# Kernel optimization log

Measured on AMD Instinct MI355X. Metric: run time of the kernel, lower is better.

## Reference

```python
import jax, jax.numpy as jnp
import numpy as np

N_GENE, N_CT, N_REF, N_SAMPLE = 50000, 64, 16, 1024

def setup_inputs() -> dict:
    key = jax.random.key(0)
    k1, k2, k3, k4, k5, k6 = jax.random.split(key, 6)
    x = jax.random.normal(k1, (N_GENE * N_CT * N_REF,), dtype=jnp.float32)
    idx = jax.random.randint(k2, (N_CT, N_GENE), 0, N_CT * N_GENE)
    # RefCombLayer weight: uniform around 1/n_ref
    num = 1.0 / N_REF
    w_ref = jax.random.uniform(k3, (N_REF * N_CT,), minval=num - num / 5, maxval=num + num / 5, dtype=jnp.float32)
    # CelltypeScaleLayer weight: normal(1.0, 0.1)
    w_ct = 1.0 + 0.1 * jax.random.normal(k4, (N_CT,), dtype=jnp.float32)
    # StretchLayer weight: normal(1.0, 0.1)
    w_stretch = 1.0 + 0.1 * jax.random.normal(k5, (N_GENE,), dtype=jnp.float32)
    # conv1 kernel: (n_sample, 1, n_kernel), normal(1/n_ct, 0.25/n_ct)
    conv_w = (1.0 / N_CT) + (0.25 / N_CT) * jax.random.normal(k6, (N_SAMPLE, 1, N_CT), dtype=jnp.float32)
    return {"x": x, "idx": idx, "w_ref": w_ref, "w_ct": w_ct,
            "w_stretch": w_stretch, "conv_w": conv_w,
            "N_batch": 1, "N_feature": N_GENE * N_CT}


def reference(x, idx, w_ref, w_ct, w_stretch, conv_w, N_batch, N_feature):
    # RefCombLayer: elementwise mul by per-gene-tiled ref weights
    y = x * jnp.tile(w_ref, N_GENE)                       # [n_gene*n_ct*n_ref]
    # SliceSumLayer: sum over n_ref slices
    y0 = y.reshape(N_CT * N_GENE, N_REF).sum(axis=1)      # [n_ct*n_gene]
    # CelltypeScaleLayer: gather per cell type, scale, flatten transposed
    z = y0[idx] * w_ct[:, None]                           # [n_ct, n_gene]
    y1 = z.T.reshape(-1)                                  # [n_gene*n_ct], gene-major
    # StretchLayer: per-gene weight repeated n_ct times
    y2 = y1 * jnp.repeat(w_stretch, N_CT)                 # [n_gene*n_ct]
    # Conv1d(1, n_sample, kernel=n_ct, stride=n_ct) == per-gene dot with kernel
    yk = y2.reshape(N_GENE, N_CT)                         # [n_gene, n_ct]
    out = jnp.einsum('gk,sk->sg', yk, conv_w[:, 0, :])    # [n_sample, n_gene]
    return (out, y0, y1, y2)
```

## Files before the change

kernel.cpp:

```cpp
#include <hip/hip_runtime.h>

#define NG 50000
#define NCT 64
#define NREF 16
#define NS 1024
#define N0 (NCT * NG)

#define OFF_Y0 ((size_t)NS * NG)
#define OFF_Y1 (OFF_Y0 + N0)
#define OFF_Y2 (OFF_Y1 + N0)

typedef __attribute__((ext_vector_type(8))) short bf16x8;
typedef __attribute__((ext_vector_type(4))) float f32x4;
typedef __attribute__((ext_vector_type(4))) unsigned short u16x4;

__device__ __forceinline__ unsigned short f2bf(float f) {
    union { float f; unsigned u; } v; v.f = f;
    unsigned r = v.u + 0x7fff + ((v.u >> 16) & 1);
    return (unsigned short)(r >> 16);
}
__device__ __forceinline__ float bf2f(unsigned short b) {
    union { float f; unsigned u; } v; v.u = ((unsigned)b) << 16;
    return v.f;
}

__global__ __launch_bounds__(256) void k_y0(const float* __restrict__ x,
                                            const float* __restrict__ w_ref,
                                            float* __restrict__ y0) {
    __shared__ f32x4 wl[256];
    const int tid = threadIdx.x;
    wl[tid] = reinterpret_cast<const f32x4*>(w_ref)[tid];
    __syncthreads();
    const int row = tid & 63;
    const f32x4 w0 = wl[row * 4 + 0];
    const f32x4 w1 = wl[row * 4 + 1];
    const f32x4 w2 = wl[row * 4 + 2];
    const f32x4 w3 = wl[row * 4 + 3];
    const f32x4* x4 = reinterpret_cast<const f32x4*>(x);
    const size_t stride = (size_t)gridDim.x * 256;
    for (size_t j = (size_t)blockIdx.x * 256 + tid; j < (size_t)N0; j += stride) {
        const f32x4* xp = x4 + j * 4;
        f32x4 a = __builtin_nontemporal_load(xp + 0);
        f32x4 b = __builtin_nontemporal_load(xp + 1);
        f32x4 c = __builtin_nontemporal_load(xp + 2);
        f32x4 d = __builtin_nontemporal_load(xp + 3);
        float s = a.x * w0.x + a.y * w0.y + a.z * w0.z + a.w * w0.w
                + b.x * w1.x + b.y * w1.y + b.z * w1.z + b.w * w1.w
                + c.x * w2.x + c.y * w2.y + c.z * w2.z + c.w * w2.w
                + d.x * w3.x + d.y * w3.y + d.z * w3.z + d.w * w3.w;
        y0[j] = s;
    }
}

__global__ __launch_bounds__(256) void k_cw(const float* __restrict__ cw,
                                            unsigned short* __restrict__ cwhi,
                                            unsigned short* __restrict__ cwlo) {
    int i = (blockIdx.x * 256 + threadIdx.x) * 4;
    f32x4 v = *reinterpret_cast<const f32x4*>(cw + i);
    u16x4 h, l;
#pragma unroll
    for (int e = 0; e < 4; ++e) {
        unsigned short hh = f2bf(v[e]);
        h[e] = hh;
        l[e] = f2bf(v[e] - bf2f(hh));
    }
    *reinterpret_cast<u16x4*>(cwhi + i) = h;
    *reinterpret_cast<u16x4*>(cwlo + i) = l;
}

#define STILE 128
template<bool PRECONV>
__global__ __launch_bounds__(256) void k_fused(const float* __restrict__ y0,
                                               const int* __restrict__ idx,
                                               const float* __restrict__ w_ct,
                                               const float* __restrict__ w_stretch,
                                               const float* __restrict__ cw,
                                               const unsigned short* __restrict__ cwhi,
                                               const unsigned short* __restrict__ cwlo,
                                               float* __restrict__ y1,
                                               float* __restrict__ y2,
                                               float* __restrict__ out) {
    __shared__ float T[64 * 65];
    __shared__ unsigned short Yhi[64 * 72];
    __shared__ unsigned short Ylo[64 * 72];

    const int tid = threadIdx.x;
    const int g0 = blockIdx.x * 64;

    int ids[16];
#pragma unroll
    for (int k = 0; k < 16; ++k) {
        int lin = k * 256 + tid;
        int c = lin >> 6, gl = lin & 63;
        int gc = min(g0 + gl, NG - 1);
        ids[k] = idx[c * NG + gc];
    }
    float vals[16];
#pragma unroll
    for (int k = 0; k < 16; ++k) vals[k] = y0[ids[k]];
#pragma unroll
    for (int k = 0; k < 16; ++k) {
        int lin = k * 256 + tid;
        int c = lin >> 6, gl = lin & 63;
        T[c * 65 + gl] = vals[k];
    }
    __syncthreads();

#pragma unroll
    for (int k = 0; k < 16; ++k) {
        int lin = k * 256 + tid;
        int gl = lin >> 6, c = lin & 63;
        int g = g0 + gl;
        float t = T[c * 65 + gl];
        float v1 = t * w_ct[c];
        float v2 = v1 * w_stretch[min(g, NG - 1)];
        int base = gl * 72 + c;
        unsigned short h = f2bf(v2);
        Yhi[base] = h;
        Ylo[base] = f2bf(v2 - bf2f(h));
        if (g < NG) {
            size_t o = (size_t)g * 64 + c;
            __builtin_nontemporal_store(v1, y1 + o);
            __builtin_nontemporal_store(v2, y2 + o);
        }
    }
    __syncthreads();

    const int lane = tid & 63;
    const int wid  = tid >> 6;
    const int l15  = lane & 15;
    const int l4   = lane >> 4;
    const int nb   = wid * 32;

    bf16x8 Ah[4][2], Al[4][2];
#pragma unroll
    for (int m = 0; m < 4; ++m) {
        int grow = m * 16 + l15;
#pragma unroll
        for (int ks = 0; ks < 2; ++ks) {
            int koff = ks * 32 + l4 * 8;
            Ah[m][ks] = *reinterpret_cast<const bf16x8*>(&Yhi[grow * 72 + koff]);
            Al[m][ks] = *reinterpret_cast<const bf16x8*>(&Ylo[grow * 72 + koff]);
        }
    }

    for (int s0 = 0; s0 < NS; s0 += STILE) {
        f32x4 acc[4][2];
#pragma unroll
        for (int m = 0; m < 4; ++m)
#pragma unroll
            for (int n = 0; n < 2; ++n) acc[m][n] = (f32x4){0.f, 0.f, 0.f, 0.f};

#pragma unroll
        for (int n = 0; n < 2; ++n) {
            const size_t srow = (size_t)(s0 + nb + n * 16 + l15) * 64;
            bf16x8 Bh[2], Bl[2];
#pragma unroll
            for (int ks = 0; ks < 2; ++ks) {
                int koff = ks * 32 + l4 * 8;
                if (PRECONV) {
                    Bh[ks] = *reinterpret_cast<const bf16x8*>(cwhi + srow + koff);
                    Bl[ks] = *reinterpret_cast<const bf16x8*>(cwlo + srow + koff);
                } else {
                    f32x4 va = *reinterpret_cast<const f32x4*>(cw + srow + koff);
                    f32x4 vb = *reinterpret_cast<const f32x4*>(cw + srow + koff + 4);
#pragma unroll
                    for (int e = 0; e < 4; ++e) {
                        unsigned short h = f2bf(va[e]);
                        Bh[ks][e] = (short)h;
                        Bl[ks][e] = (short)f2bf(va[e] - bf2f(h));
                        h = f2bf(vb[e]);
                        Bh[ks][e + 4] = (short)h;
                        Bl[ks][e + 4] = (short)f2bf(vb[e] - bf2f(h));
                    }
                }
            }
#pragma unroll
            for (int m = 0; m < 4; ++m)
#pragma unroll
                for (int ks = 0; ks < 2; ++ks) {
                    acc[m][n] = __builtin_amdgcn_mfma_f32_16x16x32_bf16(Ah[m][ks], Bh[ks], acc[m][n], 0, 0, 0);
                    acc[m][n] = __builtin_amdgcn_mfma_f32_16x16x32_bf16(Ah[m][ks], Bl[ks], acc[m][n], 0, 0, 0);
                    acc[m][n] = __builtin_amdgcn_mfma_f32_16x16x32_bf16(Al[m][ks], Bh[ks], acc[m][n], 0, 0, 0);
                }
        }

#pragma unroll
        for (int m = 0; m < 4; ++m) {
            int g4 = g0 + m * 16 + l4 * 4;
            if (g4 < NG) {
#pragma unroll
                for (int n = 0; n < 2; ++n) {
                    int s = s0 + nb + n * 16 + l15;
                    __builtin_nontemporal_store(acc[m][n], reinterpret_cast<f32x4*>(out + (size_t)s * NG + g4));
                }
            }
        }
    }
}

extern "C" void kernel_launch(void* const* d_in, const int* in_sizes, int n_in,
                              void* d_out, int out_size, void* d_ws, size_t ws_size,
                              hipStream_t stream) {
    const float* x         = (const float*)d_in[0];
    const int*   idx       = (const int*)d_in[1];
    const float* w_ref     = (const float*)d_in[2];
    const float* w_ct      = (const float*)d_in[3];
    const float* w_stretch = (const float*)d_in[4];
    const float* conv_w    = (const float*)d_in[5];

    float* out = (float*)d_out;
    float* y0  = out + OFF_Y0;
    float* y1  = out + OFF_Y1;
    float* y2  = out + OFF_Y2;

    k_y0<<<2048, 256, 0, stream>>>(x, w_ref, y0);

    const bool preconv = (ws_size >= (size_t)NS * NCT * 2 * sizeof(unsigned short));
    unsigned short* cwhi = (unsigned short*)d_ws;
    unsigned short* cwlo = cwhi + NS * NCT;
    if (preconv) {
        k_cw<<<NS * NCT / 1024, 256, 0, stream>>>(conv_w, cwhi, cwlo);
        k_fused<true><<<(NG + 63) / 64, 256, 0, stream>>>(y0, idx, w_ct, w_stretch, conv_w,
                                                          cwhi, cwlo, y1, y2, out);
    } else {
        k_fused<false><<<(NG + 63) / 64, 256, 0, stream>>>(y0, idx, w_ct, w_stretch, conv_w,
                                                           cwhi, cwlo, y1, y2, out);
    }
}
```

Before: 187.4 us.

## Split fused gather+conv kernel into separate gather and MFMA conv kernels

Splits the fused kernel in two. The first kernel does the gather and scaling, writes y1 and y2, and writes the bf16 hi/lo split of the conv operand to a workspace. The second kernel loads those A fragments straight from global memory and runs the MFMA conv with no LDS and no barriers. This is meant to free the conv kernel from the latency of the random gather and from LDS use, so it gets higher occupancy. In exchange it adds an extra kernel launch and a round trip through global memory of about 12.8 MB, and it needs a larger workspace, otherwise it falls back to the fused path.

New measurement: 204.9 us. 9.4% more time.

```diff
diff --git a/kernel.cpp b/kernel.cpp
--- a/kernel.cpp
+++ b/kernel.cpp
@@ -5,6 +5,7 @@
 #define NREF 16
 #define NS 1024
 #define N0 (NCT * NG)
+#define NGP 50048
 
 #define OFF_Y0 ((size_t)NS * NG)
 #define OFF_Y1 (OFF_Y0 + N0)
@@ -68,25 +69,136 @@
     *reinterpret_cast<u16x4*>(cwlo + i) = l;
 }
 
+__global__ __launch_bounds__(256) void k_gather2(const float* __restrict__ y0,
+                                                 const int* __restrict__ idx,
+                                                 const float* __restrict__ w_ct,
+                                                 const float* __restrict__ w_stretch,
+                                                 float* __restrict__ y1,
+                                                 float* __restrict__ y2,
+                                                 unsigned short* __restrict__ ahi,
+                                                 unsigned short* __restrict__ alo) {
+    __shared__ float T[64 * 65];
+    const int tid = threadIdx.x;
+    const int g0 = blockIdx.x * 64;
+
+    int ids[16];
+#pragma unroll
+    for (int k = 0; k < 16; ++k) {
+        int lin = k * 256 + tid;
+        int c = lin >> 6, gl = lin & 63;
+        int gc = min(g0 + gl, NG - 1);
+        ids[k] = idx[c * NG + gc];
+    }
+    float vals[16];
+#pragma unroll
+    for (int k = 0; k < 16; ++k) vals[k] = y0[ids[k]];
+#pragma unroll
+    for (int k = 0; k < 16; ++k) {
+        int lin = k * 256 + tid;
+        int c = lin >> 6, gl = lin & 63;
+        T[c * 65 + gl] = vals[k];
+    }
+    __syncthreads();
+
+#pragma unroll
+    for (int k = 0; k < 16; ++k) {
+        int lin = k * 256 + tid;
+        int gl = lin >> 6, c = lin & 63;
+        int g = g0 + gl;
+        float t = T[c * 65 + gl];
+        float v1 = t * w_ct[c];
+        float v2 = v1 * w_stretch[min(g, NG - 1)];
+        size_t o = (size_t)g * 64 + c;
+        unsigned short h = f2bf(v2);
+        ahi[o] = h;
+        alo[o] = f2bf(v2 - bf2f(h));
+        if (g < NG) {
+            __builtin_nontemporal_store(v1, y1 + o);
+            __builtin_nontemporal_store(v2, y2 + o);
+        }
+    }
+}
+
 #define STILE 128
-template<bool PRECONV>
-__global__ __launch_bounds__(256) void k_fused(const float* __restrict__ y0,
-                                               const int* __restrict__ idx,
-                                               const float* __restrict__ w_ct,
-                                               const float* __restrict__ w_stretch,
-                                               const float* __restrict__ cw,
+__global__ __launch_bounds__(256) void k_conv2(const unsigned short* __restrict__ ahi,
+                                               const unsigned short* __restrict__ alo,
                                                const unsigned short* __restrict__ cwhi,
                                                const unsigned short* __restrict__ cwlo,
-                                               float* __restrict__ y1,
-                                               float* __restrict__ y2,
                                                float* __restrict__ out) {
+    const int tid = threadIdx.x;
+    const int g0 = blockIdx.x * 64;
+    const int lane = tid & 63;
+    const int wid  = tid >> 6;
+    const int l15  = lane & 15;
+    const int l4   = lane >> 4;
+    const int nb   = wid * 32;
+
+    bf16x8 Ah[4][2], Al[4][2];
+#pragma unroll
+    for (int m = 0; m < 4; ++m) {
+        size_t grow = (size_t)(g0 + m * 16 + l15) * 64;
+#pragma unroll
+        for (int ks = 0; ks < 2; ++ks) {
+            int koff = ks * 32 + l4 * 8;
+            Ah[m][ks] = __builtin_nontemporal_load(reinterpret_cast<const bf16x8*>(ahi + grow + koff));
+            Al[m][ks] = __builtin_nontemporal_load(reinterpret_cast<const bf16x8*>(alo + grow + koff));
+        }
+    }
+
+    for (int s0 = 0; s0 < NS; s0 += STILE) {
+        f32x4 acc[4][2];
+#pragma unroll
+        for (int m = 0; m < 4; ++m)
+#pragma unroll
+            for (int n = 0; n < 2; ++n) acc[m][n] = (f32x4){0.f, 0.f, 0.f, 0.f};
+
+#pragma unroll
+        for (int n = 0; n < 2; ++n) {
+            const size_t srow = (size_t)(s0 + nb + n * 16 + l15) * 64;
+            bf16x8 Bh[2], Bl[2];
+#pragma unroll
+            for (int ks = 0; ks < 2; ++ks) {
+                int koff = ks * 32 + l4 * 8;
+                Bh[ks] = *reinterpret_cast<const bf16x8*>(cwhi + srow + koff);
+                Bl[ks] = *reinterpret_cast<const bf16x8*>(cwlo + srow + koff);
+            }
+#pragma unroll
+            for (int m = 0; m < 4; ++m)
+#pragma unroll
+                for (int ks = 0; ks < 2; ++ks) {
+                    acc[m][n] = __builtin_amdgcn_mfma_f32_16x16x32_bf16(Ah[m][ks], Bh[ks], acc[m][n], 0, 0, 0);
+                    acc[m][n] = __builtin_amdgcn_mfma_f32_16x16x32_bf16(Ah[m][ks], Bl[ks], acc[m][n], 0, 0, 0);
+                    acc[m][n] = __builtin_amdgcn_mfma_f32_16x16x32_bf16(Al[m][ks], Bh[ks], acc[m][n], 0, 0, 0);
+                }
+        }
+
+#pragma unroll
+        for (int m = 0; m < 4; ++m) {
+            int g4 = g0 + m * 16 + l4 * 4;
+            if (g4 < NG) {
+#pragma unroll
+                for (int n = 0; n < 2; ++n) {
+                    int s = s0 + nb + n * 16 + l15;
+                    __builtin_nontemporal_store(acc[m][n], reinterpret_cast<f32x4*>(out + (size_t)s * NG + g4));
+                }
+            }
+        }
+    }
+}
+
+__global__ __launch_bounds__(256) void k_fused_fb(const float* __restrict__ y0,
+                                                  const int* __restrict__ idx,
+                                                  const float* __restrict__ w_ct,
+                                                  const float* __restrict__ w_stretch,
+                                                  const float* __restrict__ cw,
+                                                  float* __restrict__ y1,
+                                                  float* __restrict__ y2,
+                                                  float* __restrict__ out) {
     __shared__ float T[64 * 65];
     __shared__ unsigned short Yhi[64 * 72];
     __shared__ unsigned short Ylo[64 * 72];
-
     const int tid = threadIdx.x;
     const int g0 = blockIdx.x * 64;
-
     int ids[16];
 #pragma unroll
     for (int k = 0; k < 16; ++k) {
@@ -105,7 +217,6 @@
         T[c * 65 + gl] = vals[k];
     }
     __syncthreads();
-
 #pragma unroll
     for (int k = 0; k < 16; ++k) {
         int lin = k * 256 + tid;
@@ -125,13 +236,11 @@
         }
     }
     __syncthreads();
-
     const int lane = tid & 63;
     const int wid  = tid >> 6;
     const int l15  = lane & 15;
     const int l4   = lane >> 4;
     const int nb   = wid * 32;
-
     bf16x8 Ah[4][2], Al[4][2];
 #pragma unroll
     for (int m = 0; m < 4; ++m) {
@@ -143,14 +252,12 @@
             Al[m][ks] = *reinterpret_cast<const bf16x8*>(&Ylo[grow * 72 + koff]);
         }
     }
-
     for (int s0 = 0; s0 < NS; s0 += STILE) {
         f32x4 acc[4][2];
 #pragma unroll
         for (int m = 0; m < 4; ++m)
 #pragma unroll
             for (int n = 0; n < 2; ++n) acc[m][n] = (f32x4){0.f, 0.f, 0.f, 0.f};
-
 #pragma unroll
         for (int n = 0; n < 2; ++n) {
             const size_t srow = (size_t)(s0 + nb + n * 16 + l15) * 64;
@@ -158,21 +265,16 @@
 #pragma unroll
             for (int ks = 0; ks < 2; ++ks) {
                 int koff = ks * 32 + l4 * 8;
-                if (PRECONV) {
-                    Bh[ks] = *reinterpret_cast<const bf16x8*>(cwhi + srow + koff);
-                    Bl[ks] = *reinterpret_cast<const bf16x8*>(cwlo + srow + koff);
-                } else {
-                    f32x4 va = *reinterpret_cast<const f32x4*>(cw + srow + koff);
-                    f32x4 vb = *reinterpret_cast<const f32x4*>(cw + srow + koff + 4);
-#pragma unroll
-                    for (int e = 0; e < 4; ++e) {
-                        unsigned short h = f2bf(va[e]);
-                        Bh[ks][e] = (short)h;
-                        Bl[ks][e] = (short)f2bf(va[e] - bf2f(h));
-                        h = f2bf(vb[e]);
-                        Bh[ks][e + 4] = (short)h;
-                        Bl[ks][e + 4] = (short)f2bf(vb[e] - bf2f(h));
-                    }
+                f32x4 va = *reinterpret_cast<const f32x4*>(cw + srow + koff);
+                f32x4 vb = *reinterpret_cast<const f32x4*>(cw + srow + koff + 4);
+#pragma unroll
+                for (int e = 0; e < 4; ++e) {
+                    unsigned short h = f2bf(va[e]);
+                    Bh[ks][e] = (short)h;
+                    Bl[ks][e] = (short)f2bf(va[e] - bf2f(h));
+                    h = f2bf(vb[e]);
+                    Bh[ks][e + 4] = (short)h;
+                    Bl[ks][e + 4] = (short)f2bf(vb[e] - bf2f(h));
                 }
             }
 #pragma unroll
@@ -184,7 +286,6 @@
                     acc[m][n] = __builtin_amdgcn_mfma_f32_16x16x32_bf16(Al[m][ks], Bh[ks], acc[m][n], 0, 0, 0);
                 }
         }
-
 #pragma unroll
         for (int m = 0; m < 4; ++m) {
             int g4 = g0 + m * 16 + l4 * 4;
@@ -216,15 +317,17 @@
 
     k_y0<<<2048, 256, 0, stream>>>(x, w_ref, y0);
 
-    const bool preconv = (ws_size >= (size_t)NS * NCT * 2 * sizeof(unsigned short));
-    unsigned short* cwhi = (unsigned short*)d_ws;
-    unsigned short* cwlo = cwhi + NS * NCT;
-    if (preconv) {
+    const size_t aplane = (size_t)NGP * NCT;
+    const size_t need = (2 * aplane + 2 * (size_t)NS * NCT) * sizeof(unsigned short);
+    if (ws_size >= need) {
+        unsigned short* ahi  = (unsigned short*)d_ws;
+        unsigned short* alo  = ahi + aplane;
+        unsigned short* cwhi = alo + aplane;
+        unsigned short* cwlo = cwhi + (size_t)NS * NCT;
         k_cw<<<NS * NCT / 1024, 256, 0, stream>>>(conv_w, cwhi, cwlo);
-        k_fused<true><<<(NG + 63) / 64, 256, 0, stream>>>(y0, idx, w_ct, w_stretch, conv_w,
-                                                          cwhi, cwlo, y1, y2, out);
+        k_gather2<<<NGP / 64, 256, 0, stream>>>(y0, idx, w_ct, w_stretch, y1, y2, ahi, alo);
+        k_conv2<<<NGP / 64, 256, 0, stream>>>(ahi, alo, cwhi, cwlo, out);
     } else {
-        k_fused<false><<<(NG + 63) / 64, 256, 0, stream>>>(y0, idx, w_ct, w_stretch, conv_w,
-                                                           cwhi, cwlo, y1, y2, out);
-    }
-}
+        k_fused_fb<<<NGP / 64, 256, 0, stream>>>(y0, idx, w_ct, w_stretch, conv_w, y1, y2, out);
+    }
+}
```

## Warp-specialize fused kernel into gather producers and MFMA consumers with double buffering

Applied to the files above, without the earlier changes.

Replaces the conv-weight preconversion kernel and the fused kernel with one 512-thread kernel. Four waves gather and scale y0 into y1/y2 and bf16 hi/lo tiles, split into two 32-gene halves. Four other waves run the split-bf16 MFMA matmul and stream `out`, so the second half's gather can overlap the first half's compute. The aim is to hide gather latency behind the output-store phase and drop one launch. In exchange, the conv weights are now converted to bf16 hi/lo inside the inner loop on every pass, which adds VALU work, and each MFMA wave covers fewer genes per B load.

Measured after the change: 185.4 us. Within noise of the previous version (-1.1%).

```diff
diff --git a/kernel.cpp b/kernel.cpp
--- a/kernel.cpp
+++ b/kernel.cpp
@@ -12,7 +12,6 @@
 
 typedef __attribute__((ext_vector_type(8))) short bf16x8;
 typedef __attribute__((ext_vector_type(4))) float f32x4;
-typedef __attribute__((ext_vector_type(4))) unsigned short u16x4;
 
 __device__ __forceinline__ unsigned short f2bf(float f) {
     union { float f; unsigned u; } v; v.f = f;
@@ -52,149 +51,129 @@
     }
 }
 
-__global__ __launch_bounds__(256) void k_cw(const float* __restrict__ cw,
-                                            unsigned short* __restrict__ cwhi,
-                                            unsigned short* __restrict__ cwlo) {
-    int i = (blockIdx.x * 256 + threadIdx.x) * 4;
-    f32x4 v = *reinterpret_cast<const f32x4*>(cw + i);
-    u16x4 h, l;
-#pragma unroll
-    for (int e = 0; e < 4; ++e) {
-        unsigned short hh = f2bf(v[e]);
-        h[e] = hh;
-        l[e] = f2bf(v[e] - bf2f(hh));
-    }
-    *reinterpret_cast<u16x4*>(cwhi + i) = h;
-    *reinterpret_cast<u16x4*>(cwlo + i) = l;
-}
+__global__ __launch_bounds__(512) void k_pc(const float* __restrict__ y0,
+                                            const int* __restrict__ idx,
+                                            const float* __restrict__ w_ct,
+                                            const float* __restrict__ w_stretch,
+                                            const float* __restrict__ cw,
+                                            float* __restrict__ y1,
+                                            float* __restrict__ y2,
+                                            float* __restrict__ out) {
+    __shared__ float T[4][64 * 9];
+    __shared__ unsigned short Phi[2][32 * 72];
+    __shared__ unsigned short Plo[2][32 * 72];
 
-#define STILE 128
-template<bool PRECONV>
-__global__ __launch_bounds__(256) void k_fused(const float* __restrict__ y0,
-                                               const int* __restrict__ idx,
-                                               const float* __restrict__ w_ct,
-                                               const float* __restrict__ w_stretch,
-                                               const float* __restrict__ cw,
-                                               const unsigned short* __restrict__ cwhi,
-                                               const unsigned short* __restrict__ cwlo,
-                                               float* __restrict__ y1,
-                                               float* __restrict__ y2,
-                                               float* __restrict__ out) {
-    __shared__ float T[64 * 65];
-    __shared__ unsigned short Yhi[64 * 72];
-    __shared__ unsigned short Ylo[64 * 72];
-
-    const int tid = threadIdx.x;
-    const int g0 = blockIdx.x * 64;
-
-    int ids[16];
-#pragma unroll
-    for (int k = 0; k < 16; ++k) {
-        int lin = k * 256 + tid;
-        int c = lin >> 6, gl = lin & 63;
-        int gc = min(g0 + gl, NG - 1);
-        ids[k] = idx[c * NG + gc];
-    }
-    float vals[16];
-#pragma unroll
-    for (int k = 0; k < 16; ++k) vals[k] = y0[ids[k]];
-#pragma unroll
-    for (int k = 0; k < 16; ++k) {
-        int lin = k * 256 + tid;
-        int c = lin >> 6, gl = lin & 63;
-        T[c * 65 + gl] = vals[k];
-    }
-    __syncthreads();
-
-#pragma unroll
-    for (int k = 0; k < 16; ++k) {
-        int lin = k * 256 + tid;
-        int gl = lin >> 6, c = lin & 63;
-        int g = g0 + gl;
-        float t = T[c * 65 + gl];
-        float v1 = t * w_ct[c];
-        float v2 = v1 * w_stretch[min(g, NG - 1)];
-        int base = gl * 72 + c;
-        unsigned short h = f2bf(v2);
-        Yhi[base] = h;
-        Ylo[base] = f2bf(v2 - bf2f(h));
-        if (g < NG) {
-            size_t o = (size_t)g * 64 + c;
-            __builtin_nontemporal_store(v1, y1 + o);
-            __builtin_nontemporal_store(v2, y2 + o);
-        }
-    }
-    __syncthreads();
-
+    const int tid  = threadIdx.x;
     const int lane = tid & 63;
     const int wid  = tid >> 6;
-    const int l15  = lane & 15;
-    const int l4   = lane >> 4;
-    const int nb   = wid * 32;
+    const int g0   = blockIdx.x * 64;
 
-    bf16x8 Ah[4][2], Al[4][2];
+    if (wid < 4) {
+        const int p = wid;
+        const float wct = w_ct[lane];
+        float* Tp = T[p];
+        for (int h = 0; h < 2; ++h) {
+            const int gbase = g0 + 32 * h + p * 8;
+            int iids[8];
 #pragma unroll
-    for (int m = 0; m < 4; ++m) {
-        int grow = m * 16 + l15;
+            for (int k = 0; k < 8; ++k) {
+                int j = lane & 7;
+                int c = (lane >> 3) + k * 8;
+                int g = min(gbase + j, NG - 1);
+                iids[k] = idx[c * NG + g];
+            }
+            float vals[8];
 #pragma unroll
-        for (int ks = 0; ks < 2; ++ks) {
-            int koff = ks * 32 + l4 * 8;
-            Ah[m][ks] = *reinterpret_cast<const bf16x8*>(&Yhi[grow * 72 + koff]);
-            Al[m][ks] = *reinterpret_cast<const bf16x8*>(&Ylo[grow * 72 + koff]);
+            for (int k = 0; k < 8; ++k) vals[k] = y0[iids[k]];
+#pragma unroll
+            for (int k = 0; k < 8; ++k) {
+                int j = lane & 7;
+                int c = (lane >> 3) + k * 8;
+                Tp[c * 9 + j] = vals[k];
+            }
+#pragma unroll
+            for (int j = 0; j < 8; ++j) {
+                int g = gbase + j;
+                float t = Tp[lane * 9 + j];
+                float v1 = t * wct;
+                float v2 = v1 * w_stretch[min(g, NG - 1)];
+                int base = (p * 8 + j) * 72 + lane;
+                unsigned short hh = f2bf(v2);
+                Phi[h][base] = hh;
+                Plo[h][base] = f2bf(v2 - bf2f(hh));
+                if (g < NG) {
+                    size_t o = (size_t)g * 64 + lane;
+                    __builtin_nontemporal_store(v1, y1 + o);
+                    __builtin_nontemporal_store(v2, y2 + o);
+                }
+            }
+            __syncthreads();
         }
-    }
-
-    for (int s0 = 0; s0 < NS; s0 += STILE) {
-        f32x4 acc[4][2];
+    } else {
+        const int cwv = wid - 4;
+        const int l15 = lane & 15;
+        const int l4  = lane >> 4;
+        __syncthreads();
+        for (int h = 0; h < 2; ++h) {
+            bf16x8 Ah[2][2], Al[2][2];
 #pragma unroll
-        for (int m = 0; m < 4; ++m)
+            for (int m = 0; m < 2; ++m) {
+                int grow = m * 16 + l15;
 #pragma unroll
-            for (int n = 0; n < 2; ++n) acc[m][n] = (f32x4){0.f, 0.f, 0.f, 0.f};
-
+                for (int ks = 0; ks < 2; ++ks) {
+                    int koff = ks * 32 + l4 * 8;
+                    Ah[m][ks] = *reinterpret_cast<const bf16x8*>(&Phi[h][grow * 72 + koff]);
+                    Al[m][ks] = *reinterpret_cast<const bf16x8*>(&Plo[h][grow * 72 + koff]);
+                }
+            }
+            const int gh = g0 + 32 * h;
+            for (int s0 = 0; s0 < NS; s0 += 128) {
+                f32x4 acc[2][2];
 #pragma unroll
-        for (int n = 0; n < 2; ++n) {
-            const size_t srow = (size_t)(s0 + nb + n * 16 + l15) * 64;
-            bf16x8 Bh[2], Bl[2];
+                for (int m = 0; m < 2; ++m)
 #pragma unroll
-            for (int ks = 0; ks < 2; ++ks) {
-                int koff = ks * 32 + l4 * 8;
-                if (PRECONV) {
-                    Bh[ks] = *reinterpret_cast<const bf16x8*>(cwhi + srow + koff);
-                    Bl[ks] = *reinterpret_cast<const bf16x8*>(cwlo + srow + koff);
-                } else {
-                    f32x4 va = *reinterpret_cast<const f32x4*>(cw + srow + koff);
-                    f32x4 vb = *reinterpret_cast<const f32x4*>(cw + srow + koff + 4);
+                    for (int n = 0; n < 2; ++n) acc[m][n] = (f32x4){0.f, 0.f, 0.f, 0.f};
 #pragma unroll
-                    for (int e = 0; e < 4; ++e) {
-                        unsigned short h = f2bf(va[e]);
-                        Bh[ks][e] = (short)h;
-                        Bl[ks][e] = (short)f2bf(va[e] - bf2f(h));
-                        h = f2bf(vb[e]);
-                        Bh[ks][e + 4] = (short)h;
-                        Bl[ks][e + 4] = (short)f2bf(vb[e] - bf2f(h));
+                for (int n = 0; n < 2; ++n) {
+                    const size_t srow = (size_t)(s0 + cwv * 32 + n * 16 + l15) * 64;
+                    bf16x8 Bh[2], Bl[2];
+#pragma unroll
+                    for (int ks = 0; ks < 2; ++ks) {
+                        int koff = ks * 32 + l4 * 8;
+                        f32x4 va = *reinterpret_cast<const f32x4*>(cw + srow + koff);
+                        f32x4 vb = *reinterpret_cast<const f32x4*>(cw + srow + koff + 4);
+#pragma unroll
+                        for (int e = 0; e < 4; ++e) {
+                            unsigned short hv = f2bf(va[e]);
+                            Bh[ks][e] = (short)hv;
+                            Bl[ks][e] = (short)f2bf(va[e] - bf2f(hv));
+                            hv = f2bf(vb[e]);
+                            Bh[ks][e + 4] = (short)hv;
+                            Bl[ks][e + 4] = (short)f2bf(vb[e] - bf2f(hv));
+                        }
+                    }
+#pragma unroll
+                    for (int m = 0; m < 2; ++m)
+#pragma unroll
+                        for (int ks = 0; ks < 2; ++ks) {
+                            acc[m][n] = __builtin_amdgcn_mfma_f32_16x16x32_bf16(Ah[m][ks], Bh[ks], acc[m][n], 0, 0, 0);
+                            acc[m][n] = __builtin_amdgcn_mfma_f32_16x16x32_bf16(Ah[m][ks], Bl[ks], acc[m][n], 0, 0, 0);
+                            acc[m][n] = __builtin_amdgcn_mfma_f32_16x16x32_bf16(Al[m][ks], Bh[ks], acc[m][n], 0, 0, 0);
+                        }
+                }
+#pragma unroll
+                for (int m = 0; m < 2; ++m) {
+                    int g4 = gh + m * 16 + l4 * 4;
+                    if (g4 < NG) {
+#pragma unroll
+                        for (int n = 0; n < 2; ++n) {
+                            int s = s0 + cwv * 32 + n * 16 + l15;
+                            __builtin_nontemporal_store(acc[m][n], reinterpret_cast<f32x4*>(out + (size_t)s * NG + g4));
+                        }
                     }
                 }
             }
-#pragma unroll
-            for (int m = 0; m < 4; ++m)
-#pragma unroll
-                for (int ks = 0; ks < 2; ++ks) {
-                    acc[m][n] = __builtin_amdgcn_mfma_f32_16x16x32_bf16(Ah[m][ks], Bh[ks], acc[m][n], 0, 0, 0);
-                    acc[m][n] = __builtin_amdgcn_mfma_f32_16x16x32_bf16(Ah[m][ks], Bl[ks], acc[m][n], 0, 0, 0);
-                    acc[m][n] = __builtin_amdgcn_mfma_f32_16x16x32_bf16(Al[m][ks], Bh[ks], acc[m][n], 0, 0, 0);
-                }
-        }
-
-#pragma unroll
-        for (int m = 0; m < 4; ++m) {
-            int g4 = g0 + m * 16 + l4 * 4;
-            if (g4 < NG) {
-#pragma unroll
-                for (int n = 0; n < 2; ++n) {
-                    int s = s0 + nb + n * 16 + l15;
-                    __builtin_nontemporal_store(acc[m][n], reinterpret_cast<f32x4*>(out + (size_t)s * NG + g4));
-                }
-            }
+            if (h == 0) __syncthreads();
         }
     }
 }
@@ -215,16 +194,5 @@
     float* y2  = out + OFF_Y2;
 
     k_y0<<<2048, 256, 0, stream>>>(x, w_ref, y0);
-
-    const bool preconv = (ws_size >= (size_t)NS * NCT * 2 * sizeof(unsigned short));
-    unsigned short* cwhi = (unsigned short*)d_ws;
-    unsigned short* cwlo = cwhi + NS * NCT;
-    if (preconv) {
-        k_cw<<<NS * NCT / 1024, 256, 0, stream>>>(conv_w, cwhi, cwlo);
-        k_fused<true><<<(NG + 63) / 64, 256, 0, stream>>>(y0, idx, w_ct, w_stretch, conv_w,
-                                                          cwhi, cwlo, y1, y2, out);
-    } else {
-        k_fused<false><<<(NG + 63) / 64, 256, 0, stream>>>(y0, idx, w_ct, w_stretch, conv_w,
-                                                           cwhi, cwlo, y1, y2, out);
-    }
+    k_pc<<<(NG + 63) / 64, 512, 0, stream>>>(y0, idx, w_ct, w_stretch, conv_w, y1, y2, out);
 }
```

## Split fused gather/conv kernel into separate gather and conv kernels

Applied to the files above, without the earlier changes.

Splits the fused gather-scale-and-conv kernel into two launches. The first writes y1 and y2, and the second re-reads y2 from global memory, converting both y2 and conv_w to hi/lo bf16 in registers. This also drops the separate conv_w preconversion kernel and the workspace path. It is meant to cut LDS use and register pressure in the conv kernel so occupancy rises. In exchange it re-reads y2 (about 12.8 MB, likely from cache since the nontemporal store just wrote it) and redoes the conv_w conversion in every block.

Measured after the change: 190.5 us. Within noise of the previous version (+1.6%).

```diff
diff --git a/kernel.cpp b/kernel.cpp
--- a/kernel.cpp
+++ b/kernel.cpp
@@ -12,7 +12,6 @@
 
 typedef __attribute__((ext_vector_type(8))) short bf16x8;
 typedef __attribute__((ext_vector_type(4))) float f32x4;
-typedef __attribute__((ext_vector_type(4))) unsigned short u16x4;
 
 __device__ __forceinline__ unsigned short f2bf(float f) {
     union { float f; unsigned u; } v; v.f = f;
@@ -52,38 +51,13 @@
     }
 }
 
-__global__ __launch_bounds__(256) void k_cw(const float* __restrict__ cw,
-                                            unsigned short* __restrict__ cwhi,
-                                            unsigned short* __restrict__ cwlo) {
-    int i = (blockIdx.x * 256 + threadIdx.x) * 4;
-    f32x4 v = *reinterpret_cast<const f32x4*>(cw + i);
-    u16x4 h, l;
-#pragma unroll
-    for (int e = 0; e < 4; ++e) {
-        unsigned short hh = f2bf(v[e]);
-        h[e] = hh;
-        l[e] = f2bf(v[e] - bf2f(hh));
-    }
-    *reinterpret_cast<u16x4*>(cwhi + i) = h;
-    *reinterpret_cast<u16x4*>(cwlo + i) = l;
-}
-
-#define STILE 128
-template<bool PRECONV>
-__global__ __launch_bounds__(256) void k_fused(const float* __restrict__ y0,
-                                               const int* __restrict__ idx,
-                                               const float* __restrict__ w_ct,
-                                               const float* __restrict__ w_stretch,
-                                               const float* __restrict__ cw,
-                                               const unsigned short* __restrict__ cwhi,
-                                               const unsigned short* __restrict__ cwlo,
-                                               float* __restrict__ y1,
-                                               float* __restrict__ y2,
-                                               float* __restrict__ out) {
+__global__ __launch_bounds__(256) void k_gather2(const float* __restrict__ y0,
+                                                 const int* __restrict__ idx,
+                                                 const float* __restrict__ w_ct,
+                                                 const float* __restrict__ w_stretch,
+                                                 float* __restrict__ y1,
+                                                 float* __restrict__ y2) {
     __shared__ float T[64 * 65];
-    __shared__ unsigned short Yhi[64 * 72];
-    __shared__ unsigned short Ylo[64 * 72];
-
     const int tid = threadIdx.x;
     const int g0 = blockIdx.x * 64;
 
@@ -111,21 +85,23 @@
         int lin = k * 256 + tid;
         int gl = lin >> 6, c = lin & 63;
         int g = g0 + gl;
-        float t = T[c * 65 + gl];
-        float v1 = t * w_ct[c];
-        float v2 = v1 * w_stretch[min(g, NG - 1)];
-        int base = gl * 72 + c;
-        unsigned short h = f2bf(v2);
-        Yhi[base] = h;
-        Ylo[base] = f2bf(v2 - bf2f(h));
         if (g < NG) {
+            float t = T[c * 65 + gl];
+            float v1 = t * w_ct[c];
+            float v2 = v1 * w_stretch[g];
             size_t o = (size_t)g * 64 + c;
             __builtin_nontemporal_store(v1, y1 + o);
             __builtin_nontemporal_store(v2, y2 + o);
         }
     }
-    __syncthreads();
-
+}
+
+#define STILE 128
+__global__ __launch_bounds__(256) void k_conv2(const float* __restrict__ y2,
+                                               const float* __restrict__ cw,
+                                               float* __restrict__ out) {
+    const int tid  = threadIdx.x;
+    const int g0   = blockIdx.x * 64;
     const int lane = tid & 63;
     const int wid  = tid >> 6;
     const int l15  = lane & 15;
@@ -135,12 +111,21 @@
     bf16x8 Ah[4][2], Al[4][2];
 #pragma unroll
     for (int m = 0; m < 4; ++m) {
-        int grow = m * 16 + l15;
+        size_t row = (size_t)min(g0 + m * 16 + l15, NG - 1) * 64;
 #pragma unroll
         for (int ks = 0; ks < 2; ++ks) {
             int koff = ks * 32 + l4 * 8;
-            Ah[m][ks] = *reinterpret_cast<const bf16x8*>(&Yhi[grow * 72 + koff]);
-            Al[m][ks] = *reinterpret_cast<const bf16x8*>(&Ylo[grow * 72 + koff]);
+            f32x4 va = *reinterpret_cast<const f32x4*>(y2 + row + koff);
+            f32x4 vb = *reinterpret_cast<const f32x4*>(y2 + row + koff + 4);
+#pragma unroll
+            for (int e = 0; e < 4; ++e) {
+                unsigned short h = f2bf(va[e]);
+                Ah[m][ks][e] = (short)h;
+                Al[m][ks][e] = (short)f2bf(va[e] - bf2f(h));
+                h = f2bf(vb[e]);
+                Ah[m][ks][e + 4] = (short)h;
+                Al[m][ks][e + 4] = (short)f2bf(vb[e] - bf2f(h));
+            }
         }
     }
 
@@ -158,21 +143,16 @@
 #pragma unroll
             for (int ks = 0; ks < 2; ++ks) {
                 int koff = ks * 32 + l4 * 8;
-                if (PRECONV) {
-                    Bh[ks] = *reinterpret_cast<const bf16x8*>(cwhi + srow + koff);
-                    Bl[ks] = *reinterpret_cast<const bf16x8*>(cwlo + srow + koff);
-                } else {
-                    f32x4 va = *reinterpret_cast<const f32x4*>(cw + srow + koff);
-                    f32x4 vb = *reinterpret_cast<const f32x4*>(cw + srow + koff + 4);
-#pragma unroll
-                    for (int e = 0; e < 4; ++e) {
-                        unsigned short h = f2bf(va[e]);
-                        Bh[ks][e] = (short)h;
-                        Bl[ks][e] = (short)f2bf(va[e] - bf2f(h));
-                        h = f2bf(vb[e]);
-                        Bh[ks][e + 4] = (short)h;
-                        Bl[ks][e + 4] = (short)f2bf(vb[e] - bf2f(h));
-                    }
+                f32x4 va = *reinterpret_cast<const f32x4*>(cw + srow + koff);
+                f32x4 vb = *reinterpret_cast<const f32x4*>(cw + srow + koff + 4);
+#pragma unroll
+                for (int e = 0; e < 4; ++e) {
+                    unsigned short h = f2bf(va[e]);
+                    Bh[ks][e] = (short)h;
+                    Bl[ks][e] = (short)f2bf(va[e] - bf2f(h));
+                    h = f2bf(vb[e]);
+                    Bh[ks][e + 4] = (short)h;
+                    Bl[ks][e + 4] = (short)f2bf(vb[e] - bf2f(h));
                 }
             }
 #pragma unroll
@@ -215,16 +195,6 @@
     float* y2  = out + OFF_Y2;
 
     k_y0<<<2048, 256, 0, stream>>>(x, w_ref, y0);
-
-    const bool preconv = (ws_size >= (size_t)NS * NCT * 2 * sizeof(unsigned short));
-    unsigned short* cwhi = (unsigned short*)d_ws;
-    unsigned short* cwlo = cwhi + NS * NCT;
-    if (preconv) {
-        k_cw<<<NS * NCT / 1024, 256, 0, stream>>>(conv_w, cwhi, cwlo);
-        k_fused<true><<<(NG + 63) / 64, 256, 0, stream>>>(y0, idx, w_ct, w_stretch, conv_w,
-                                                          cwhi, cwlo, y1, y2, out);
-    } else {
-        k_fused<false><<<(NG + 63) / 64, 256, 0, stream>>>(y0, idx, w_ct, w_stretch, conv_w,
-                                                           cwhi, cwlo, y1, y2, out);
-    }
-}
+    k_gather2<<<(NG + 63) / 64, 256, 0, stream>>>(y0, idx, w_ct, w_stretch, y1, y2);
+    k_conv2<<<(NG + 63) / 64, 256, 0, stream>>>(y2, conv_w, out);
+}
```
